# Kernel optimization log

Hardware: AMD Instinct MI355X
Metric: run time of the kernel (lower is better)

Reference implementation:

```python
import jax, jax.numpy as jnp
import numpy as np

D_MODEL = 1024
N_HEADS = 16
D_K = D_MODEL // N_HEADS  # 64
THETA = 10000.0


def _rope(x, token_positions):
    # x: [b, h, s, d], token_positions: [s]
    inv_freq = 1.0 / THETA ** (jnp.arange(0, D_K, 2, dtype=jnp.float32) / D_K)  # [d/2]
    ang = token_positions.astype(jnp.float32)[:, None] * inv_freq               # [s, d/2]
    cos, sin = jnp.cos(ang), jnp.sin(ang)                                       # broadcast over b,h
    x1 = x[..., 0::2]
    x2 = x[..., 1::2]
    even = x1 * cos - x2 * sin
    odd = x1 * sin + x2 * cos
    return jnp.stack([even, odd], axis=-1).reshape(x.shape)  # re-interleave


def setup_inputs() -> dict:
    key = jax.random.key(0)
    k1, k2, k3 = jax.random.split(key, 3)
    B, S = 2, 2048
    x = jax.random.normal(k1, (B, S, D_MODEL), dtype=jnp.float32)
    token_positions = jnp.arange(S, dtype=jnp.int32)
    std_qkv = np.sqrt(2.0 / (D_MODEL + 3 * D_MODEL))
    std_out = np.sqrt(2.0 / (D_MODEL + D_MODEL))
    W_qkv = jax.random.normal(k2, (3 * D_MODEL, D_MODEL), dtype=jnp.float32) * std_qkv
    W_out = jax.random.normal(k3, (D_MODEL, D_MODEL), dtype=jnp.float32) * std_out
    return {"x": x, "token_positions": token_positions, "W_qkv": W_qkv, "W_out": W_out}


def reference(x, token_positions, W_qkv, W_out):
    B, S, _ = x.shape
    qkv = jnp.einsum('bsi,oi->bso', x, W_qkv)                 # [b, s, 3*h*d]
    qkv = qkv.reshape(B, S, 3, N_HEADS, D_K)
    qkv = jnp.transpose(qkv, (2, 0, 3, 1, 4))                 # [3, b, h, s, d]
    q, k, v = qkv[0], qkv[1], qkv[2]
    q = _rope(q, token_positions)
    k = _rope(k, token_positions)
    scores = jnp.einsum('bhqd,bhkd->bhqk', q, k) / jnp.sqrt(jnp.float32(D_K))
    mask = jnp.tril(jnp.ones((S, S), dtype=bool))
    scores = jnp.where(mask, scores, -jnp.inf)
    attn = jax.nn.softmax(scores, axis=-1)
    out = jnp.einsum('bhqk,bhkd->bhqd', attn, v)              # [b, h, s, d]
    out = jnp.transpose(out, (0, 2, 1, 3)).reshape(B, S, D_MODEL)
    return jnp.einsum('bsi,oi->bso', out, W_out)
```

## Files before the change

### kernel.cpp

```cpp
#include <hip/hip_runtime.h>
#include <hip/hip_bf16.h>
#include <math.h>

#define D_MODEL 1024
#define N_HEADS 16
#define D_K     64
#define S_LEN   2048
#define B_SZ    2

typedef unsigned short u16;
typedef unsigned int   u32;
using short8  = __attribute__((ext_vector_type(8))) short;
using ushort8 = __attribute__((ext_vector_type(8))) unsigned short;
using f32x4   = __attribute__((ext_vector_type(4))) float;

__device__ inline float bf2f(u16 u) { return __uint_as_float((u32)u << 16); }
__device__ inline u16 f2bf(float f) {
    __hip_bfloat16 h = __float2bfloat16(f);
    return *(u16*)&h;
}
__device__ inline float fast_exp2(float x) { return __builtin_amdgcn_exp2f(x); }
__device__ inline void gload_lds16(const void* g, void* l) {
    __builtin_amdgcn_global_load_lds(
        (const __attribute__((address_space(1))) unsigned int*)g,
        (__attribute__((address_space(3))) unsigned int*)l, 16, 0, 0);
}

__global__ __launch_bounds__(256)
void cast3_f32_bf16(const float* __restrict__ a, u16* __restrict__ ao, int na4,
                    const float* __restrict__ bsrc, u16* __restrict__ bo, int nb4,
                    const float* __restrict__ c, u16* __restrict__ co, int nc4) {
    int j = blockIdx.x * 256 + threadIdx.x;
    const float* src; u16* dst;
    if (j < na4) { src = a; dst = ao; }
    else {
        j -= na4;
        if (j < nb4) { src = bsrc; dst = bo; }
        else {
            j -= nb4;
            if (j >= nc4) return;
            src = c; dst = co;
        }
    }
    float4 v = ((const float4*)src)[j];
    ushort4 u;
    u.x = f2bf(v.x); u.y = f2bf(v.y); u.z = f2bf(v.z); u.w = f2bf(v.w);
    ((ushort4*)dst)[j] = u;
}

template <bool OUT_BF16>
__global__ __launch_bounds__(256)
void gemm_bt_mfma(const u16* __restrict__ A, const u16* __restrict__ B,
                  void* __restrict__ Cout, int M, int N, int K) {
    __shared__ u16 As[2][128 * 32];
    __shared__ u16 Bs[2][128 * 32];
    const int tid  = threadIdx.x;
    const int lane = tid & 63;
    const int wv   = tid >> 6;
    const int wm   = wv >> 1, wn = wv & 1;
    const int row0 = blockIdx.y * 128;
    const int col0 = blockIdx.x * 128;

    const int lr = lane >> 2;
    const int lc = (lane & 3) * 8;

    f32x4 acc[4][4] = {};

    auto STAGE = [&](int k0, int bf) {
#pragma unroll
        for (int t = 0; t < 2; t++) {
            int rblk = wv * 32 + t * 16;
            gload_lds16(A + (size_t)(row0 + rblk + lr) * K + k0 + lc, &As[bf][rblk * 32]);
            gload_lds16(B + (size_t)(col0 + rblk + lr) * K + k0 + lc, &Bs[bf][rblk * 32]);
        }
    };

    STAGE(0, 0);
    __syncthreads();

    int cur = 0;
    for (int k0 = 0; k0 < K; k0 += 32) {
        if (k0 + 32 < K) STAGE(k0 + 32, cur ^ 1);

        short8 af[4], bfr[4];
#pragma unroll
        for (int mi = 0; mi < 4; mi++)
            af[mi] = *(const short8*)&As[cur][(wm * 64 + mi * 16 + (lane & 15)) * 32 + (lane >> 4) * 8];
#pragma unroll
        for (int nj = 0; nj < 4; nj++)
            bfr[nj] = *(const short8*)&Bs[cur][(wn * 64 + nj * 16 + (lane & 15)) * 32 + (lane >> 4) * 8];
#pragma unroll
        for (int mi = 0; mi < 4; mi++)
#pragma unroll
            for (int nj = 0; nj < 4; nj++)
                acc[mi][nj] = __builtin_amdgcn_mfma_f32_16x16x32_bf16(
                    af[mi], bfr[nj], acc[mi][nj], 0, 0, 0);

        __syncthreads();
        cur ^= 1;
    }

    const int cr = (lane >> 4) * 4;
    const int cc = lane & 15;
#pragma unroll
    for (int mi = 0; mi < 4; mi++) {
#pragma unroll
        for (int nj = 0; nj < 4; nj++) {
            int c = col0 + wn * 64 + nj * 16 + cc;
#pragma unroll
            for (int r = 0; r < 4; r++) {
                int rr = row0 + wm * 64 + mi * 16 + cr + r;
                if (OUT_BF16)
                    ((u16*)Cout)[(size_t)rr * N + c] = f2bf(acc[mi][nj][r]);
                else
                    ((float*)Cout)[(size_t)rr * N + c] = acc[mi][nj][r];
            }
        }
    }
}

__global__ __launch_bounds__(256)
void gemm_bt_mfma_64r(const u16* __restrict__ A, const u16* __restrict__ B,
                      float* __restrict__ Cout, int M, int N, int K) {
    __shared__ u16 As[2][64 * 32];
    __shared__ u16 Bs[2][128 * 32];
    const int tid  = threadIdx.x;
    const int lane = tid & 63;
    const int wv   = tid >> 6;
    const int wm   = wv >> 1, wn = wv & 1;
    const int row0 = blockIdx.y * 64;
    const int col0 = blockIdx.x * 128;

    const int lr = lane >> 2;
    const int lc = (lane & 3) * 8;

    f32x4 acc[2][4] = {};

    auto STAGE = [&](int k0, int bf) {
        gload_lds16(A + (size_t)(row0 + wv * 16 + lr) * K + k0 + lc, &As[bf][(wv * 16) * 32]);
#pragma unroll
        for (int t = 0; t < 2; t++) {
            int rblk = wv * 32 + t * 16;
            gload_lds16(B + (size_t)(col0 + rblk + lr) * K + k0 + lc, &Bs[bf][rblk * 32]);
        }
    };

    STAGE(0, 0);
    __syncthreads();

    int cur = 0;
    for (int k0 = 0; k0 < K; k0 += 32) {
        if (k0 + 32 < K) STAGE(k0 + 32, cur ^ 1);

        short8 af[2], bfr[4];
#pragma unroll
        for (int mi = 0; mi < 2; mi++)
            af[mi] = *(const short8*)&As[cur][(wm * 32 + mi * 16 + (lane & 15)) * 32 + (lane >> 4) * 8];
#pragma unroll
        for (int nj = 0; nj < 4; nj++)
            bfr[nj] = *(const short8*)&Bs[cur][(wn * 64 + nj * 16 + (lane & 15)) * 32 + (lane >> 4) * 8];
#pragma unroll
        for (int mi = 0; mi < 2; mi++)
#pragma unroll
            for (int nj = 0; nj < 4; nj++)
                acc[mi][nj] = __builtin_amdgcn_mfma_f32_16x16x32_bf16(
                    af[mi], bfr[nj], acc[mi][nj], 0, 0, 0);

        __syncthreads();
        cur ^= 1;
    }

    const int cr = (lane >> 4) * 4;
    const int cc = lane & 15;
#pragma unroll
    for (int mi = 0; mi < 2; mi++) {
#pragma unroll
        for (int nj = 0; nj < 4; nj++) {
            int c = col0 + wn * 64 + nj * 16 + cc;
#pragma unroll
            for (int r = 0; r < 4; r++) {
                int rr = row0 + wm * 32 + mi * 16 + cr + r;
                Cout[(size_t)rr * N + c] = acc[mi][nj][r];
            }
        }
    }
}

__global__ __launch_bounds__(256)
void prep_vtrans_rope(u16* __restrict__ qkv, u16* __restrict__ VT,
                      const int* __restrict__ pos) {
    const int bid = blockIdx.x;
    const int tid = threadIdx.x;

    if (bid < 1024) {
        __shared__ u16 t[64][68];
        const int st = bid & 31, h = (bid >> 5) & 15, b = bid >> 9;
        const int bh = b * N_HEADS + h;
#pragma unroll
        for (int i = 0; i < 4; i++) {
            int e  = tid + i * 256;
            int sl = e >> 4;
            int c4 = e & 15;
            ushort4 v = *(const ushort4*)&qkv[((size_t)(b * S_LEN + st * 64 + sl) * 3 + 2) * D_MODEL
                                              + h * D_K + c4 * 4];
            *(ushort4*)&t[sl][c4 * 4] = v;
        }
        __syncthreads();
#pragma unroll
        for (int i = 0; i < 4; i++) {
            int e  = tid + i * 256;
            int d  = e >> 4;
            int s4 = e & 15;
            ushort4 o;
            o.x = t[s4 * 4 + 0][d];
            o.y = t[s4 * 4 + 1][d];
            o.z = t[s4 * 4 + 2][d];
            o.w = t[s4 * 4 + 3][d];
            *(ushort4*)&VT[((size_t)bh * D_K + d) * S_LEN + st * 64 + s4 * 4] = o;
        }
        return;
    }

    int e  = (bid - 1024) * 256 + tid;
    int j8 = e & 7;
    int h  = (e >> 3) & 15;
    int w  = (e >> 7) & 1;
    int s  = (e >> 8) & 2047;
    int b  = e >> 19;

    float p  = (float)pos[s];
    float sc = (w == 0) ? 0.18033688011112042f : 1.0f;

    size_t base = (((size_t)(b * S_LEN + s) * 3 + w) * D_MODEL) + h * D_K + j8 * 8;
    ushort8 v = *(const ushort8*)&qkv[base];

    const float C = -0.41524101186092056f;
#pragma unroll
    for (int jj = 0; jj < 4; jj++) {
        int j = j8 * 4 + jj;
        float ang = p * fast_exp2((float)j * C);
        float sn, cs;
        __sincosf(ang, &sn, &cs);
        float x1 = bf2f(v[2 * jj]);
        float x2 = bf2f(v[2 * jj + 1]);
        v[2 * jj]     = f2bf((x1 * cs - x2 * sn) * sc);
        v[2 * jj + 1] = f2bf((x1 * sn + x2 * cs) * sc);
    }
    *(ushort8*)&qkv[base] = v;
}

__device__ __forceinline__ void attn_step(
    const u16* __restrict__ Ksc, const u16* __restrict__ Vsc,
    u16* __restrict__ Psw,
    short8 (&qf)[2], f32x4 (&acc)[4], float& mq, float& lq,
    int k0, int qw0, bool diag, int l15, int quad, int qsw)
{
    f32x4 s[4] = {};
    __builtin_amdgcn_s_setprio(1);
#pragma unroll
    for (int kf = 0; kf < 2; kf++)
#pragma unroll
        for (int nj = 0; nj < 4; nj++) {
            short8 kfr = *(const short8*)&Ksc[kf * 2048 + (nj * 16 + l15) * 32 + qsw * 8];
            s[nj] = __builtin_amdgcn_mfma_f32_16x16x32_bf16(kfr, qf[kf], s[nj], 0, 0, 0);
        }
    __builtin_amdgcn_s_setprio(0);

    if (diag) {
        const int row_g = qw0 + l15;
#pragma unroll
        for (int nj = 0; nj < 4; nj++)
#pragma unroll
            for (int r = 0; r < 4; r++) {
                int key_g = k0 + nj * 16 + quad * 4 + r;
                if (key_g > row_g) s[nj][r] = -INFINITY;
            }
    }

    float rmax = s[0][0];
#pragma unroll
    for (int nj = 0; nj < 4; nj++)
#pragma unroll
        for (int r = 0; r < 4; r++) rmax = fmaxf(rmax, s[nj][r]);
    rmax = fmaxf(rmax, __shfl_xor(rmax, 16, 64));
    rmax = fmaxf(rmax, __shfl_xor(rmax, 32, 64));

    if (!__all(rmax <= mq + 12.f)) {
        float mn = fmaxf(mq, rmax);
        float alpha = fast_exp2(mq - mn);
        mq = mn;
        lq *= alpha;
#pragma unroll
        for (int nj = 0; nj < 4; nj++)
#pragma unroll
            for (int r = 0; r < 4; r++) acc[nj][r] *= alpha;
    }

    float rsum = 0.f;
#pragma unroll
    for (int nj = 0; nj < 4; nj++)
#pragma unroll
        for (int r = 0; r < 4; r++) {
            float p = fast_exp2(s[nj][r] - mq);
            s[nj][r] = p;
            rsum += p;
        }
    rsum += __shfl_xor(rsum, 16, 64);
    rsum += __shfl_xor(rsum, 32, 64);
    lq += rsum;

#pragma unroll
    for (int nj = 0; nj < 4; nj++) {
        u32 lo = ((u32)f2bf(s[nj][1]) << 16) | f2bf(s[nj][0]);
        u32 hi = ((u32)f2bf(s[nj][3]) << 16) | f2bf(s[nj][2]);
        uint2 pk; pk.x = lo; pk.y = hi;
        *(uint2*)&Psw[l15 * 68 + nj * 16 + quad * 4] = pk;
    }

    __builtin_amdgcn_s_setprio(1);
#pragma unroll
    for (int kf = 0; kf < 2; kf++) {
        const u16* pp = &Psw[l15 * 68 + kf * 32 + quad * 8];
        uint2 plo = *(const uint2*)pp;
        uint2 phi = *(const uint2*)(pp + 4);
        u32 praw[4] = { plo.x, plo.y, phi.x, phi.y };
        short8 pf = *(const short8*)praw;
#pragma unroll
        for (int nj = 0; nj < 4; nj++) {
            short8 vf = *(const short8*)&Vsc[kf * 2048 + (nj * 16 + l15) * 32 + qsw * 8];
            acc[nj] = __builtin_amdgcn_mfma_f32_16x16x32_bf16(vf, pf, acc[nj], 0, 0, 0);
        }
    }
    __builtin_amdgcn_s_setprio(0);
}

__global__ __launch_bounds__(256)
void attn_mfma(const u16* __restrict__ qkv, const u16* __restrict__ VT,
               u16* __restrict__ out, float* __restrict__ partO,
               float* __restrict__ partML) {
    __shared__ u16 Ks[2][64 * 32];
    __shared__ u16 VsT[2][64 * 32];
    __shared__ u16 Ps[4][16 * 68];

    const int tid  = threadIdx.x;
    const int lane = tid & 63;
    const int wv   = tid >> 6;

    const int bid  = blockIdx.x;
    const int idx  = bid >> 3;
    const int bh   = (bid & 7) * 4 + (idx >> 5);
    const int rem  = idx & 31;
    const int pr   = rem >> 1;
    const int role = rem & 1;
    const int qtH  = 31 - pr;
    const int qtL  = pr;
    const int h    = bh & (N_HEADS - 1);
    const int b    = bh >> 4;

    const int l15  = lane & 15;
    const int quad = lane >> 4;
    const int qsw  = quad ^ ((l15 >> 1) & 3);
    const int qw0H = qtH * 64 + wv * 16;

    const size_t vtb = (size_t)bh * D_K * S_LEN;
    u16* Psw = &Ps[wv][0];
    const int lr  = lane >> 2;
    const int csw = ((lane & 3) ^ ((lane >> 3) & 3)) * 8;

    auto STAGE = [&](int kts) {
        const int k0s = kts * 64;
#pragma unroll
        for (int kf = 0; kf < 2; kf++)
            gload_lds16(qkv + ((size_t)(b * S_LEN + k0s + wv * 16 + lr) * 3 + 1) * D_MODEL
                            + h * D_K + kf * 32 + csw,
                        &Ks[kf][(wv * 16) * 32]);
#pragma unroll
        for (int kc = 0; kc < 2; kc++)
            gload_lds16(VT + vtb + (size_t)(wv * 16 + lr) * S_LEN + k0s + kc * 32 + csw,
                        &VsT[kc][(wv * 16) * 32]);
    };

    ushort8 kreg[2], vreg[2];
    auto REGLOAD = [&](int kts) {
        const int k0s = kts * 64;
#pragma unroll
        for (int kf = 0; kf < 2; kf++)
            kreg[kf] = *(const ushort8*)&qkv[((size_t)(b * S_LEN + k0s + wv * 16 + lr) * 3 + 1) * D_MODEL
                                             + h * D_K + kf * 32 + csw];
#pragma unroll
        for (int kc = 0; kc < 2; kc++)
            vreg[kc] = *(const ushort8*)&VT[vtb + (size_t)(wv * 16 + lr) * S_LEN + k0s + kc * 32 + csw];
    };
    auto LDSW = [&]() {
#pragma unroll
        for (int kf = 0; kf < 2; kf++)
            *(ushort8*)&Ks[kf][(wv * 16) * 32 + lane * 8] = kreg[kf];
#pragma unroll
        for (int kc = 0; kc < 2; kc++)
            *(ushort8*)&VsT[kc][(wv * 16) * 32 + lane * 8] = vreg[kc];
    };

    short8 qfH[2];
#pragma unroll
    for (int kf = 0; kf < 2; kf++)
        qfH[kf] = *(const short8*)&qkv[((size_t)(b * S_LEN + qw0H + l15) * 3 + 0) * D_MODEL
                                       + h * D_K + kf * 32 + quad * 8];
    f32x4 accH[4] = {};
    float mqH = -INFINITY, lqH = 0.f;

    const int kbeg = role ? 17 : 0;
    const int kend = role ? qtH : 16;
    if (kbeg <= kend) {
        STAGE(kbeg);
        __syncthreads();
        for (int kt = kbeg; kt <= kend; kt++) {
            const bool more = kt < kend;
            if (more) REGLOAD(kt + 1);
            attn_step(&Ks[0][0], &VsT[0][0], Psw, qfH, accH, mqH, lqH,
                      kt * 64, qw0H, kt == qtH, l15, quad, qsw);
            __syncthreads();
            if (more) { LDSW(); __syncthreads(); }
        }
    }

    {
        const size_t unit = (size_t)(bh * 16 + (qtH - 16)) * 2 + role;
        float* Od = partO + unit * 4096 + (size_t)(wv * 16 + l15) * 64;
#pragma unroll
        for (int nj = 0; nj < 4; nj++)
            *(f32x4*)&Od[nj * 16 + quad * 4] = accH[nj];
        if (quad == 0) {
            float* ML = partML + unit * 128;
            ML[wv * 16 + l15]      = mqH;
            ML[64 + wv * 16 + l15] = lqH;
        }
    }

    if (!role) return;

    const int qw0L = qtL * 64 + wv * 16;
    short8 qfL[2];
#pragma unroll
    for (int kf = 0; kf < 2; kf++)
        qfL[kf] = *(const short8*)&qkv[((size_t)(b * S_LEN + qw0L + l15) * 3 + 0) * D_MODEL
                                       + h * D_K + kf * 32 + quad * 8];
    f32x4 accL[4] = {};
    float mqL = -INFINITY, lqL = 0.f;

    STAGE(0);
    __syncthreads();
    for (int kt = 0; kt <= qtL; kt++) {
        const bool more = kt < qtL;
        if (more) REGLOAD(kt + 1);
        attn_step(&Ks[0][0], &VsT[0][0], Psw, qfL, accL, mqL, lqL,
                  kt * 64, qw0L, kt == qtL, l15, quad, qsw);
        __syncthreads();
        if (more) { LDSW(); __syncthreads(); }
    }

    float invl = 1.f / lqL;
#pragma unroll
    for (int nj = 0; nj < 4; nj++) {
        ushort4 o;
        o.x = f2bf(accL[nj][0] * invl); o.y = f2bf(accL[nj][1] * invl);
        o.z = f2bf(accL[nj][2] * invl); o.w = f2bf(accL[nj][3] * invl);
        *(ushort4*)&out[(size_t)(b * S_LEN + qw0L + l15) * D_MODEL
                        + h * D_K + nj * 16 + quad * 4] = o;
    }
}

__global__ __launch_bounds__(256)
void attn_combine(const float* __restrict__ partO, const float* __restrict__ partML,
                  u16* __restrict__ out) {
    const int t16 = blockIdx.x & 15;
    const int bh  = blockIdx.x >> 4;
    const int h = bh & (N_HEADS - 1), b = bh >> 4;
    const int q0 = (t16 + 16) * 64;
    const int tid = threadIdx.x;
    const int q  = tid >> 2;
    const int d0 = (tid & 3) * 16;

    const size_t u0 = (size_t)(bh * 16 + t16) * 2;
    const float* O0 = partO + u0 * 4096;
    const float* O1 = O0 + 4096;
    const float* ML0 = partML + u0 * 128;
    const float* ML1 = ML0 + 128;

    float m0 = ML0[q], l0 = ML0[64 + q];
    float m1 = ML1[q], l1 = ML1[64 + q];
    float ms = fmaxf(m0, m1);
    float f0 = fast_exp2(m0 - ms), f1 = fast_exp2(m1 - ms);
    float inv = 1.f / (l0 * f0 + l1 * f1);
    f0 *= inv; f1 *= inv;
#pragma unroll
    for (int i = 0; i < 4; i++) {
        float4 a = *(const float4*)&O0[q * 64 + d0 + i * 4];
        float4 c = *(const float4*)&O1[q * 64 + d0 + i * 4];
        ushort4 o;
        o.x = f2bf(a.x * f0 + c.x * f1);
        o.y = f2bf(a.y * f0 + c.y * f1);
        o.z = f2bf(a.z * f0 + c.z * f1);
        o.w = f2bf(a.w * f0 + c.w * f1);
        *(ushort4*)&out[(size_t)(b * S_LEN + q0 + q) * D_MODEL + h * D_K + d0 + i * 4] = o;
    }
}

extern "C" void kernel_launch(void* const* d_in, const int* in_sizes, int n_in,
                              void* d_out, int out_size, void* d_ws, size_t ws_size,
                              hipStream_t stream) {
    const float* x    = (const float*)d_in[0];
    const int*   pos  = (const int*)d_in[1];
    const float* Wqkv = (const float*)d_in[2];
    const float* Wout = (const float*)d_in[3];
    float*       out  = (float*)d_out;

    const int M = B_SZ * S_LEN;

    u16* qkvb = (u16*)d_ws;
    u16* aob  = qkvb + (size_t)M * 3 * D_MODEL;
    u16* xb   = aob  + (size_t)M * D_MODEL;
    u16* wqb  = xb   + (size_t)M * D_MODEL;
    u16* wob  = wqb  + (size_t)3 * D_MODEL * D_MODEL;
    u16* vtb  = wob  + (size_t)D_MODEL * D_MODEL;
    float* partO  = (float*)(vtb + (size_t)M * D_MODEL);
    float* partML = partO + (size_t)1024 * 4096;

    const int na4 = M * D_MODEL / 4;
    const int nb4 = 3 * D_MODEL * D_MODEL / 4;
    const int nc4 = D_MODEL * D_MODEL / 4;
    cast3_f32_bf16<<<(na4 + nb4 + nc4 + 255) / 256, 256, 0, stream>>>(
        x, xb, na4, Wqkv, wqb, nb4, Wout, wob, nc4);

    gemm_bt_mfma<true><<<dim3(3 * D_MODEL / 128, M / 128), 256, 0, stream>>>(
        xb, wqb, qkvb, M, 3 * D_MODEL, D_MODEL);

    prep_vtrans_rope<<<5120, 256, 0, stream>>>(qkvb, vtb, pos);

    attn_mfma<<<1024, 256, 0, stream>>>(qkvb, vtb, aob, partO, partML);
    attn_combine<<<512, 256, 0, stream>>>(partO, partML, aob);

    gemm_bt_mfma_64r<<<dim3(D_MODEL / 128, M / 64), 256, 0, stream>>>(
        aob, wob, out, M, D_MODEL, D_MODEL);
}
```

Measured before the change: 185.7 us.

## Fuse RoPE and query scaling into QKV GEMM epilogue; split V transpose kernel

Applies rotary embedding and the query scale directly in the QKV GEMM epilogue, computing each value's interleaved partner with a lane shuffle. This avoids rereading and rewriting the Q/K halves of the qkv buffer in a separate pass. The V transpose becomes its own smaller kernel. The attention softmax max and sum reductions are also restructured as trees to shorten dependency chains. The epilogue now does sincos per output element, which adds ALU work inside the GEMM, and RoPE is applied to fp32 accumulators before the bf16 rounding.

```diff
diff --git a/kernel.cpp b/kernel.cpp
--- a/kernel.cpp
+++ b/kernel.cpp
@@ -48,10 +48,10 @@
     ((ushort4*)dst)[j] = u;
 }
 
-template <bool OUT_BF16>
 __global__ __launch_bounds__(256)
-void gemm_bt_mfma(const u16* __restrict__ A, const u16* __restrict__ B,
-                  void* __restrict__ Cout, int M, int N, int K) {
+void gemm_qkv_rope(const u16* __restrict__ A, const u16* __restrict__ B,
+                   u16* __restrict__ Cout, const int* __restrict__ pos,
+                   int M, int N, int K) {
     __shared__ u16 As[2][128 * 32];
     __shared__ u16 Bs[2][128 * 32];
     const int tid  = threadIdx.x;
@@ -102,18 +102,35 @@
 
     const int cr = (lane >> 4) * 4;
     const int cc = lane & 15;
+    const int cb = col0 + wn * 64 + cc;
+    const int w  = cb >> 10;
+    const float CLOG = -0.41524101186092056f;
+    const float qsc  = (w == 0) ? 0.18033688011112042f : 1.0f;
+    float invf[4];
+#pragma unroll
+    for (int nj = 0; nj < 4; nj++)
+        invf[nj] = fast_exp2((float)(((cb + nj * 16) & 63) >> 1) * CLOG);
+
 #pragma unroll
     for (int mi = 0; mi < 4; mi++) {
 #pragma unroll
-        for (int nj = 0; nj < 4; nj++) {
-            int c = col0 + wn * 64 + nj * 16 + cc;
-#pragma unroll
-            for (int r = 0; r < 4; r++) {
-                int rr = row0 + wm * 64 + mi * 16 + cr + r;
-                if (OUT_BF16)
-                    ((u16*)Cout)[(size_t)rr * N + c] = f2bf(acc[mi][nj][r]);
-                else
-                    ((float*)Cout)[(size_t)rr * N + c] = acc[mi][nj][r];
+        for (int r = 0; r < 4; r++) {
+            int rr = row0 + wm * 64 + mi * 16 + cr + r;
+            float p = (w == 2) ? 0.f : (float)pos[rr & (S_LEN - 1)];
+#pragma unroll
+            for (int nj = 0; nj < 4; nj++) {
+                float v = acc[mi][nj][r];
+                float partner = __shfl_xor(v, 1, 64);
+                float res;
+                if (w == 2) {
+                    res = v;
+                } else {
+                    float sn, cs;
+                    __sincosf(p * invf[nj], &sn, &cs);
+                    res = ((cc & 1) ? (partner * sn + v * cs)
+                                    : (v * cs - partner * sn)) * qsc;
+                }
+                Cout[(size_t)rr * N + cb + nj * 16] = f2bf(res);
             }
         }
     }
@@ -187,66 +204,34 @@
 }
 
 __global__ __launch_bounds__(256)
-void prep_vtrans_rope(u16* __restrict__ qkv, u16* __restrict__ VT,
-                      const int* __restrict__ pos) {
+void vtrans(const u16* __restrict__ qkv, u16* __restrict__ VT) {
+    __shared__ u16 t[64][68];
     const int bid = blockIdx.x;
     const int tid = threadIdx.x;
-
-    if (bid < 1024) {
-        __shared__ u16 t[64][68];
-        const int st = bid & 31, h = (bid >> 5) & 15, b = bid >> 9;
-        const int bh = b * N_HEADS + h;
-#pragma unroll
-        for (int i = 0; i < 4; i++) {
-            int e  = tid + i * 256;
-            int sl = e >> 4;
-            int c4 = e & 15;
-            ushort4 v = *(const ushort4*)&qkv[((size_t)(b * S_LEN + st * 64 + sl) * 3 + 2) * D_MODEL
-                                              + h * D_K + c4 * 4];
-            *(ushort4*)&t[sl][c4 * 4] = v;
-        }
-        __syncthreads();
-#pragma unroll
-        for (int i = 0; i < 4; i++) {
-            int e  = tid + i * 256;
-            int d  = e >> 4;
-            int s4 = e & 15;
-            ushort4 o;
-            o.x = t[s4 * 4 + 0][d];
-            o.y = t[s4 * 4 + 1][d];
-            o.z = t[s4 * 4 + 2][d];
-            o.w = t[s4 * 4 + 3][d];
-            *(ushort4*)&VT[((size_t)bh * D_K + d) * S_LEN + st * 64 + s4 * 4] = o;
-        }
-        return;
-    }
-
-    int e  = (bid - 1024) * 256 + tid;
-    int j8 = e & 7;
-    int h  = (e >> 3) & 15;
-    int w  = (e >> 7) & 1;
-    int s  = (e >> 8) & 2047;
-    int b  = e >> 19;
-
-    float p  = (float)pos[s];
-    float sc = (w == 0) ? 0.18033688011112042f : 1.0f;
-
-    size_t base = (((size_t)(b * S_LEN + s) * 3 + w) * D_MODEL) + h * D_K + j8 * 8;
-    ushort8 v = *(const ushort8*)&qkv[base];
-
-    const float C = -0.41524101186092056f;
-#pragma unroll
-    for (int jj = 0; jj < 4; jj++) {
-        int j = j8 * 4 + jj;
-        float ang = p * fast_exp2((float)j * C);
-        float sn, cs;
-        __sincosf(ang, &sn, &cs);
-        float x1 = bf2f(v[2 * jj]);
-        float x2 = bf2f(v[2 * jj + 1]);
-        v[2 * jj]     = f2bf((x1 * cs - x2 * sn) * sc);
-        v[2 * jj + 1] = f2bf((x1 * sn + x2 * cs) * sc);
-    }
-    *(ushort8*)&qkv[base] = v;
+    const int st = bid & 31, h = (bid >> 5) & 15, b = bid >> 9;
+    const int bh = b * N_HEADS + h;
+#pragma unroll
+    for (int i = 0; i < 4; i++) {
+        int e  = tid + i * 256;
+        int sl = e >> 4;
+        int c4 = e & 15;
+        ushort4 v = *(const ushort4*)&qkv[((size_t)(b * S_LEN + st * 64 + sl) * 3 + 2) * D_MODEL
+                                          + h * D_K + c4 * 4];
+        *(ushort4*)&t[sl][c4 * 4] = v;
+    }
+    __syncthreads();
+#pragma unroll
+    for (int i = 0; i < 4; i++) {
+        int e  = tid + i * 256;
+        int d  = e >> 4;
+        int s4 = e & 15;
+        ushort4 o;
+        o.x = t[s4 * 4 + 0][d];
+        o.y = t[s4 * 4 + 1][d];
+        o.z = t[s4 * 4 + 2][d];
+        o.w = t[s4 * 4 + 3][d];
+        *(ushort4*)&VT[((size_t)bh * D_K + d) * S_LEN + st * 64 + s4 * 4] = o;
+    }
 }
 
 __device__ __forceinline__ void attn_step(
@@ -277,11 +262,11 @@
             }
     }
 
-    float rmax = s[0][0];
+    float mx[4];
 #pragma unroll
     for (int nj = 0; nj < 4; nj++)
-#pragma unroll
-        for (int r = 0; r < 4; r++) rmax = fmaxf(rmax, s[nj][r]);
+        mx[nj] = fmaxf(fmaxf(s[nj][0], s[nj][1]), fmaxf(s[nj][2], s[nj][3]));
+    float rmax = fmaxf(fmaxf(mx[0], mx[1]), fmaxf(mx[2], mx[3]));
     rmax = fmaxf(rmax, __shfl_xor(rmax, 16, 64));
     rmax = fmaxf(rmax, __shfl_xor(rmax, 32, 64));
 
@@ -296,15 +281,17 @@
             for (int r = 0; r < 4; r++) acc[nj][r] *= alpha;
     }
 
-    float rsum = 0.f;
-#pragma unroll
-    for (int nj = 0; nj < 4; nj++)
-#pragma unroll
-        for (int r = 0; r < 4; r++) {
-            float p = fast_exp2(s[nj][r] - mq);
-            s[nj][r] = p;
-            rsum += p;
-        }
+    float rs[4];
+#pragma unroll
+    for (int nj = 0; nj < 4; nj++) {
+        float p0 = fast_exp2(s[nj][0] - mq);
+        float p1 = fast_exp2(s[nj][1] - mq);
+        float p2 = fast_exp2(s[nj][2] - mq);
+        float p3 = fast_exp2(s[nj][3] - mq);
+        s[nj][0] = p0; s[nj][1] = p1; s[nj][2] = p2; s[nj][3] = p3;
+        rs[nj] = (p0 + p1) + (p2 + p3);
+    }
+    float rsum = (rs[0] + rs[1]) + (rs[2] + rs[3]);
     rsum += __shfl_xor(rsum, 16, 64);
     rsum += __shfl_xor(rsum, 32, 64);
     lq += rsum;
@@ -531,10 +518,10 @@
     cast3_f32_bf16<<<(na4 + nb4 + nc4 + 255) / 256, 256, 0, stream>>>(
         x, xb, na4, Wqkv, wqb, nb4, Wout, wob, nc4);
 
-    gemm_bt_mfma<true><<<dim3(3 * D_MODEL / 128, M / 128), 256, 0, stream>>>(
-        xb, wqb, qkvb, M, 3 * D_MODEL, D_MODEL);
-
-    prep_vtrans_rope<<<5120, 256, 0, stream>>>(qkvb, vtb, pos);
+    gemm_qkv_rope<<<dim3(3 * D_MODEL / 128, M / 128), 256, 0, stream>>>(
+        xb, wqb, qkvb, pos, M, 3 * D_MODEL, D_MODEL);
+
+    vtrans<<<1024, 256, 0, stream>>>(qkvb, vtb);
 
     attn_mfma<<<1024, 256, 0, stream>>>(qkvb, vtb, aob, partO, partML);
     attn_combine<<<512, 256, 0, stream>>>(partO, partML, aob);
```

Result: no change. 183.3 us (-1.3%).
